# Optimization experiments

Hardware: AMD Instinct MI355X
Metric: run time of the kernel (lower is better)

Reference implementation:

```python
import jax, jax.numpy as jnp
import numpy as np

GROUP = 9  # candidates per group, from .view(B, -1, 9)


def setup_inputs() -> dict:
    key = jax.random.key(0)
    k1, k2 = jax.random.split(key)
    x1 = jax.random.normal(k1, (8, 2048, 1024), dtype=jnp.float32)
    x2 = jax.random.normal(k2, (8, 1152, 1024), dtype=jnp.float32)
    return {"x1": x1, "x2": x2}


def reference(x1, x2):
    # batch pairwise squared distances: ||a||^2 + ||b||^2 - 2 a.b  -> [B, N1, N2]
    sq1 = jnp.sum(x1 * x1, axis=-1)[:, :, None]          # [B, N1, 1]
    sq2 = jnp.sum(x2 * x2, axis=-1)[:, None, :]          # [B, 1, N2]
    cross = jnp.einsum("bnd,bmd->bnm", x1, x2)           # [B, N1, N2]
    d = sq1 + sq2 - 2.0 * cross
    # group consecutive candidates in blocks of 9, mode='min'
    B = x1.shape[0]
    d = d.reshape(B, -1, GROUP)                           # [B, N1*N2/9, 9]
    d = jnp.min(d, axis=-1)                               # [B, N1*N2/9]
    # reduce=True -> scalar mean
    return jnp.mean(d)
```

## Files before the change

### kernel.cpp

```cpp
#include <hip/hip_runtime.h>

#define NB 8
#define N1 2048
#define N2 1152
#define KD 1024
#define BM 256
#define BN 144
#define BNP 145
#define BUFB 25600
#define NBUF 3

typedef __attribute__((ext_vector_type(4))) float f32x4;
typedef __attribute__((ext_vector_type(2))) long i64x2;

__device__ __forceinline__ unsigned pack4_fp8(f32x4 v) {
  int t = __builtin_amdgcn_cvt_pk_fp8_f32(v.x, v.y, 0, false);
  t = __builtin_amdgcn_cvt_pk_fp8_f32(v.z, v.w, t, true);
  return (unsigned)t;
}

__device__ __forceinline__ void async_copy16(const void* g, void* l) {
  __builtin_amdgcn_global_load_lds(
      (const __attribute__((address_space(1))) unsigned int*)g,
      (__attribute__((address_space(3))) unsigned int*)l, 16, 0, 0);
}

__global__ __launch_bounds__(256) void convert_kernel(
    const float* __restrict__ x1, const float* __restrict__ x2,
    unsigned char* __restrict__ x1q, unsigned char* __restrict__ x2q,
    float* __restrict__ sq1, float* __restrict__ sq2,
    float* __restrict__ out) {
  __shared__ __align__(16) unsigned char lds[4096];
  if (blockIdx.x == 0 && threadIdx.x == 0) *out = 0.f;
  int wave = threadIdx.x >> 6, lane = threadIdx.x & 63;
  int bid = blockIdx.x;
  int b = bid & 7;
  int idx = bid >> 3;
  const float* src;
  unsigned char* dst;
  float* sqp;
  if (idx < N1 / 4) {
    int row = b * N1 + idx * 4 + wave;
    src = x1 + (size_t)row * KD;
    dst = x1q + (size_t)row * KD;
    sqp = sq1 + row;
  } else {
    int row = b * N2 + (idx - N1 / 4) * 4 + wave;
    src = x2 + (size_t)row * KD;
    dst = x2q + (size_t)row * KD;
    sqp = sq2 + row;
  }
  const f32x4* s4 = (const f32x4*)src;
  int r = 4 * (lane & 15);
  int q = (r & 31) >> 3;
  int h = r >> 5;
  int pos = (lane >> 4) * 64 + q * 16 + h * 8 + (r & 7);
  unsigned char* my = lds + wave * 1024;
  float s = 0.f;
#pragma unroll
  for (int i = 0; i < 4; ++i) {
    f32x4 v = __builtin_nontemporal_load(&s4[i * 64 + lane]);
    *(unsigned*)(my + i * 256 + pos) = pack4_fp8(v);
    s += v.x * v.x + v.y * v.y + v.z * v.z + v.w * v.w;
  }
  asm volatile("s_waitcnt lgkmcnt(0)" ::: "memory");
  ((uint4*)dst)[lane] = *(const uint4*)(my + lane * 16);
#pragma unroll
  for (int off = 32; off > 0; off >>= 1) s += __shfl_down(s, off);
  if (lane == 0) *sqp = s;
}

__global__ __launch_bounds__(512, 4) void dist_kernel(
    const unsigned char* __restrict__ x1q, const unsigned char* __restrict__ x2q,
    const float* __restrict__ sq1, const float* __restrict__ sq2,
    float* __restrict__ out) {
  __shared__ __align__(16) char smem[NBUF * BUFB];

  const int tid = threadIdx.x;
  const int wave = tid >> 6, lane = tid & 63;
  const int bid = blockIdx.x;
  const int b = bid & 7;
  const int bm = (bid >> 3) & 7;
  const int bn = bid >> 6;

  const unsigned char* Ag = x1q + ((size_t)b * N1 + bm * BM) * KD;
  const unsigned char* Bg = x2q + ((size_t)b * N2 + bn * BN) * KD;

  const int lr = lane >> 2, sl = lane & 3;
  const int goff = (sl ^ ((lr >> 1) & 3)) * 16;

  const int quad = lane >> 4, fr = lane & 15;
  const int fslot = (fr * 4 + (quad ^ ((fr >> 1) & 3))) * 16;

  f32x4 acc[2][9];
#pragma unroll
  for (int i = 0; i < 2; ++i)
#pragma unroll
    for (int j = 0; j < 9; ++j) {
      f32x4 z = {0.f, 0.f, 0.f, 0.f};
      acc[i][j] = z;
    }

  auto stage = [&](int buf, int k0) {
    char* base = smem + buf * BUFB;
#pragma unroll
    for (int t = 0; t < 3; ++t) {
      int j = wave * 3 + t;
      const unsigned char* g;
      if (j < 16)
        g = Ag + (size_t)(j * 16 + lr) * KD + k0 + goff;
      else
        g = Bg + (size_t)((j - 16) * 16 + lr) * KD + k0 + goff;
      async_copy16(g, base + j * 1024 + lane * 16);
    }
    async_copy16(Bg + (size_t)(128 + lr) * KD + k0 + goff,
                 base + 24 * 1024 + lane * 16);
  };

#define COMPUTE(cbp)                                                          \
  {                                                                           \
    const char* cb = (cbp);                                                   \
    i64x2 a0 = *(const i64x2*)(cb + (2 * wave + 0) * 1024 + fslot);           \
    i64x2 a1 = *(const i64x2*)(cb + (2 * wave + 1) * 1024 + fslot);           \
    __builtin_amdgcn_s_setprio(1);                                            \
    _Pragma("unroll") for (int tn = 0; tn < 9; ++tn) {                        \
      i64x2 bf = *(const i64x2*)(cb + 16384 + tn * 1024 + fslot);             \
      acc[0][tn] = __builtin_amdgcn_mfma_f32_16x16x32_fp8_fp8(                \
          a0.x, bf.x, acc[0][tn], 0, 0, 0);                                   \
      acc[0][tn] = __builtin_amdgcn_mfma_f32_16x16x32_fp8_fp8(                \
          a0.y, bf.y, acc[0][tn], 0, 0, 0);                                   \
      acc[1][tn] = __builtin_amdgcn_mfma_f32_16x16x32_fp8_fp8(                \
          a1.x, bf.x, acc[1][tn], 0, 0, 0);                                   \
      acc[1][tn] = __builtin_amdgcn_mfma_f32_16x16x32_fp8_fp8(                \
          a1.y, bf.y, acc[1][tn], 0, 0, 0);                                   \
    }                                                                         \
    __builtin_amdgcn_s_setprio(0);                                            \
  }

  stage(0, 0);
  stage(1, 64);

  int cur = 0;
  for (int i = 0; i < 15; ++i) {
    asm volatile("s_waitcnt lgkmcnt(0)" ::: "memory");
    asm volatile("s_waitcnt vmcnt(4)" ::: "memory");
    __builtin_amdgcn_s_barrier();
    __builtin_amdgcn_sched_barrier(0);
    if (i < 14) {
      int b2 = cur + 2;
      if (b2 >= NBUF) b2 -= NBUF;
      stage(b2, (i + 2) * 64);
    }
    COMPUTE(smem + cur * BUFB);
    ++cur;
    if (cur == NBUF) cur = 0;
  }
  asm volatile("s_waitcnt lgkmcnt(0)" ::: "memory");
  asm volatile("s_waitcnt vmcnt(0)" ::: "memory");
  __builtin_amdgcn_s_barrier();
  __builtin_amdgcn_sched_barrier(0);
  COMPUTE(smem + cur * BUFB);

  float s2[9];
#pragma unroll
  for (int tn = 0; tn < 9; ++tn)
    s2[tn] = sq2[(size_t)b * N2 + bn * BN + tn * 16 + fr];

  float s1v[2][4];
#pragma unroll
  for (int tm = 0; tm < 2; ++tm)
#pragma unroll
    for (int rr = 0; rr < 4; ++rr)
      s1v[tm][rr] =
          sq1[(size_t)b * N1 + bm * BM + (2 * wave + tm) * 16 + quad * 4 + rr];

  float* eps = (float*)smem;
  float local = 0.f;
#pragma unroll
  for (int tm = 0; tm < 2; ++tm) {
    __syncthreads();
#pragma unroll
    for (int tn = 0; tn < 9; ++tn)
#pragma unroll
      for (int rr = 0; rr < 4; ++rr)
        eps[(wave * 16 + quad * 4 + rr) * BNP + tn * 16 + fr] =
            s1v[tm][rr] + s2[tn] - 2.0f * acc[tm][tn][rr];
    __syncthreads();
#pragma unroll
    for (int qq = 0; qq < 4; ++qq) {
      int g = tid + qq * 512;
      int row = g >> 4, grp = g & 15;
      const float* p = eps + row * BNP + grp * 9;
      float mn = p[0];
#pragma unroll
      for (int jj = 1; jj < 9; ++jj) mn = fminf(mn, p[jj]);
      local += mn;
    }
  }

#pragma unroll
  for (int off = 32; off > 0; off >>= 1) local += __shfl_down(local, off);
  __syncthreads();
  if (lane == 0) eps[wave] = local;
  __syncthreads();
  if (tid == 0) {
    float s = 0.f;
#pragma unroll
    for (int w = 0; w < 8; ++w) s += eps[w];
    atomicAdd(out, s * (1.0f / 2097152.0f));
  }
}

extern "C" void kernel_launch(void* const* d_in, const int* in_sizes, int n_in,
                              void* d_out, int out_size, void* d_ws, size_t ws_size,
                              hipStream_t stream) {
  const float* x1 = (const float*)d_in[0];
  const float* x2 = (const float*)d_in[1];
  char* ws = (char*)d_ws;
  const size_t x1q_bytes = (size_t)NB * N1 * KD;
  const size_t x2q_bytes = (size_t)NB * N2 * KD;
  unsigned char* x1q = (unsigned char*)ws;
  unsigned char* x2q = (unsigned char*)(ws + x1q_bytes);
  float* sq1 = (float*)(ws + x1q_bytes + x2q_bytes);
  float* sq2 = (float*)(ws + x1q_bytes + x2q_bytes + (size_t)NB * N1 * 4);

  convert_kernel<<<NB * (N1 / 4 + N2 / 4), 256, 0, stream>>>(x1, x2, x1q, x2q,
                                                             sq1, sq2,
                                                             (float*)d_out);
  dist_kernel<<<NB * (N1 / BM) * (N2 / BN), 512, 0, stream>>>(x1q, x2q, sq1, sq2,
                                                              (float*)d_out);
}
```

Before: 160.9 us.

## Double K-tile depth to 128 per stage and flatten epilogue into one pass

Each pipeline stage now loads a 128-deep K slice instead of 64, which halves the number of barrier and wait iterations and doubles the MFMA work done per synchronisation. The stage issue moves inside the compute body, and the launch-bounds occupancy hint drops from 4 to 2 blocks because shared memory per block doubles to about 150 KB. The epilogue writes the full 256x144 distance tile to shared memory at once and does the group-min reduction in a single pass, which removes one pair of syncthreads. The cost is fewer resident blocks per CU, leaving less room to hide memory latency.

```diff
diff --git a/kernel.cpp b/kernel.cpp
--- a/kernel.cpp
+++ b/kernel.cpp
@@ -7,7 +7,8 @@
 #define BM 256
 #define BN 144
 #define BNP 145
-#define BUFB 25600
+#define BK 128
+#define BUFB 51200
 #define NBUF 3
 
 typedef __attribute__((ext_vector_type(4))) float f32x4;
@@ -70,7 +71,7 @@
   if (lane == 0) *sqp = s;
 }
 
-__global__ __launch_bounds__(512, 4) void dist_kernel(
+__global__ __launch_bounds__(512, 2) void dist_kernel(
     const unsigned char* __restrict__ x1q, const unsigned char* __restrict__ x2q,
     const float* __restrict__ sq1, const float* __restrict__ sq2,
     float* __restrict__ out) {
@@ -104,54 +105,60 @@
   auto stage = [&](int buf, int k0) {
     char* base = smem + buf * BUFB;
 #pragma unroll
-    for (int t = 0; t < 3; ++t) {
-      int j = wave * 3 + t;
+    for (int t = 0; t < 6; ++t) {
+      int j = wave * 6 + t;
       const unsigned char* g;
-      if (j < 16)
-        g = Ag + (size_t)(j * 16 + lr) * KD + k0 + goff;
-      else
-        g = Bg + (size_t)((j - 16) * 16 + lr) * KD + k0 + goff;
+      if (j < 32) {
+        int rc = j >> 1, kb = j & 1;
+        g = Ag + (size_t)(rc * 16 + lr) * KD + k0 + kb * 64 + goff;
+      } else {
+        int jj = j - 32;
+        int rc = jj >> 1, kb = jj & 1;
+        g = Bg + (size_t)(rc * 16 + lr) * KD + k0 + kb * 64 + goff;
+      }
       async_copy16(g, base + j * 1024 + lane * 16);
     }
     async_copy16(Bg + (size_t)(128 + lr) * KD + k0 + goff,
-                 base + 24 * 1024 + lane * 16);
+                 base + 48 * 1024 + lane * 16);
+    async_copy16(Bg + (size_t)(128 + lr) * KD + k0 + 64 + goff,
+                 base + 49 * 1024 + lane * 16);
   };
 
-#define COMPUTE(cbp)                                                          \
+#define KBODY(cbp, do_stage, knext)                                           \
   {                                                                           \
     const char* cb = (cbp);                                                   \
-    i64x2 a0 = *(const i64x2*)(cb + (2 * wave + 0) * 1024 + fslot);           \
-    i64x2 a1 = *(const i64x2*)(cb + (2 * wave + 1) * 1024 + fslot);           \
-    __builtin_amdgcn_s_setprio(1);                                            \
-    _Pragma("unroll") for (int tn = 0; tn < 9; ++tn) {                        \
-      i64x2 bf = *(const i64x2*)(cb + 16384 + tn * 1024 + fslot);             \
-      acc[0][tn] = __builtin_amdgcn_mfma_f32_16x16x32_fp8_fp8(                \
-          a0.x, bf.x, acc[0][tn], 0, 0, 0);                                   \
-      acc[0][tn] = __builtin_amdgcn_mfma_f32_16x16x32_fp8_fp8(                \
-          a0.y, bf.y, acc[0][tn], 0, 0, 0);                                   \
-      acc[1][tn] = __builtin_amdgcn_mfma_f32_16x16x32_fp8_fp8(                \
-          a1.x, bf.x, acc[1][tn], 0, 0, 0);                                   \
-      acc[1][tn] = __builtin_amdgcn_mfma_f32_16x16x32_fp8_fp8(                \
-          a1.y, bf.y, acc[1][tn], 0, 0, 0);                                   \
+    if (do_stage) {                                                           \
+      int b2 = cur + 2;                                                       \
+      if (b2 >= NBUF) b2 -= NBUF;                                             \
+      stage(b2, (knext)*BK);                                                  \
     }                                                                         \
-    __builtin_amdgcn_s_setprio(0);                                            \
+    _Pragma("unroll") for (int kb = 0; kb < 2; ++kb) {                        \
+      i64x2 a0 = *(const i64x2*)(cb + ((wave * 2 + 0) * 2 + kb) * 1024 + fslot); \
+      i64x2 a1 = *(const i64x2*)(cb + ((wave * 2 + 1) * 2 + kb) * 1024 + fslot); \
+      _Pragma("unroll") for (int tn = 0; tn < 9; ++tn) {                      \
+        i64x2 bf = *(const i64x2*)(cb + (32 + tn * 2 + kb) * 1024 + fslot);   \
+        acc[0][tn] = __builtin_amdgcn_mfma_f32_16x16x32_fp8_fp8(              \
+            a0.x, bf.x, acc[0][tn], 0, 0, 0);                                 \
+        acc[0][tn] = __builtin_amdgcn_mfma_f32_16x16x32_fp8_fp8(              \
+            a0.y, bf.y, acc[0][tn], 0, 0, 0);                                 \
+        acc[1][tn] = __builtin_amdgcn_mfma_f32_16x16x32_fp8_fp8(              \
+            a1.x, bf.x, acc[1][tn], 0, 0, 0);                                 \
+        acc[1][tn] = __builtin_amdgcn_mfma_f32_16x16x32_fp8_fp8(              \
+            a1.y, bf.y, acc[1][tn], 0, 0, 0);                                 \
+      }                                                                       \
+    }                                                                         \
   }
 
   stage(0, 0);
-  stage(1, 64);
+  stage(1, BK);
 
   int cur = 0;
-  for (int i = 0; i < 15; ++i) {
+  for (int i = 0; i < 7; ++i) {
     asm volatile("s_waitcnt lgkmcnt(0)" ::: "memory");
-    asm volatile("s_waitcnt vmcnt(4)" ::: "memory");
+    asm volatile("s_waitcnt vmcnt(8)" ::: "memory");
     __builtin_amdgcn_s_barrier();
     __builtin_amdgcn_sched_barrier(0);
-    if (i < 14) {
-      int b2 = cur + 2;
-      if (b2 >= NBUF) b2 -= NBUF;
-      stage(b2, (i + 2) * 64);
-    }
-    COMPUTE(smem + cur * BUFB);
+    KBODY(smem + cur * BUFB, (i < 6), i + 2);
     ++cur;
     if (cur == NBUF) cur = 0;
   }
@@ -159,7 +166,7 @@
   asm volatile("s_waitcnt vmcnt(0)" ::: "memory");
   __builtin_amdgcn_s_barrier();
   __builtin_amdgcn_sched_barrier(0);
-  COMPUTE(smem + cur * BUFB);
+  KBODY(smem + cur * BUFB, false, 0);
 
   float s2[9];
 #pragma unroll
@@ -172,30 +179,29 @@
 #pragma unroll
     for (int rr = 0; rr < 4; ++rr)
       s1v[tm][rr] =
-          sq1[(size_t)b * N1 + bm * BM + (2 * wave + tm) * 16 + quad * 4 + rr];
+          sq1[(size_t)b * N1 + bm * BM + wave * 32 + tm * 16 + quad * 4 + rr];
 
   float* eps = (float*)smem;
   float local = 0.f;
-#pragma unroll
-  for (int tm = 0; tm < 2; ++tm) {
-    __syncthreads();
+  __syncthreads();
+#pragma unroll
+  for (int tm = 0; tm < 2; ++tm)
 #pragma unroll
     for (int tn = 0; tn < 9; ++tn)
 #pragma unroll
       for (int rr = 0; rr < 4; ++rr)
-        eps[(wave * 16 + quad * 4 + rr) * BNP + tn * 16 + fr] =
+        eps[(wave * 32 + tm * 16 + quad * 4 + rr) * BNP + tn * 16 + fr] =
             s1v[tm][rr] + s2[tn] - 2.0f * acc[tm][tn][rr];
-    __syncthreads();
-#pragma unroll
-    for (int qq = 0; qq < 4; ++qq) {
-      int g = tid + qq * 512;
-      int row = g >> 4, grp = g & 15;
-      const float* p = eps + row * BNP + grp * 9;
-      float mn = p[0];
-#pragma unroll
-      for (int jj = 1; jj < 9; ++jj) mn = fminf(mn, p[jj]);
-      local += mn;
-    }
+  __syncthreads();
+#pragma unroll
+  for (int qq = 0; qq < 8; ++qq) {
+    int g = tid + qq * 512;
+    int row = g >> 4, grp = g & 15;
+    const float* pp = eps + row * BNP + grp * 9;
+    float mn = pp[0];
+#pragma unroll
+    for (int jj = 1; jj < 9; ++jj) mn = fminf(mn, pp[jj]);
+    local += mn;
   }
 
 #pragma unroll
```

New measurement: 156.2 us. -2.9%, faster.
